# Kernel optimization log

Measured on AMD Instinct MI355X. Metric: run time of the kernel, lower is better.

## Reference

```python
import jax, jax.numpy as jnp
import numpy as np
import math

BOUND = 1e-06
PI = math.pi

N_DIMS = 256
N_ROWS = 524288
DELTA = 1e-06


def _make_buffers(n_dims, delta, radius, scaling, range_type="bound"):
    if range_type == "whole":
        phi_L = 0.0
    else:  # 'bound'
        L = 0.01
        upper_bound = PI / 2 * (1.0 - L)
        phi_L = math.asin(delta ** (1.0 / n_dims))
        phi_L = phi_L if phi_L < upper_bound else upper_bound
    # W_theta: identity with last row duplicated -> (n_dims+1, n_dims)
    eye = np.eye(n_dims, dtype=np.float32)
    W_theta = np.concatenate([eye, eye[-1:]], axis=0)
    # W_phi: strictly upper-triangular ones, with [-2, -1] zeroed
    W_phi = np.triu(np.ones((n_dims + 1, n_dims + 1), dtype=np.float32), k=1)
    W_phi[-2, -1] = 0.0
    b_phi = np.zeros(n_dims + 1, dtype=np.float32)
    b_phi[-1] = -PI / 2.0
    return (
        jnp.float32(phi_L),
        jnp.asarray(W_theta),
        jnp.asarray(W_phi),
        jnp.asarray(b_phi),
        jnp.float32(radius),
        jnp.float32(scaling),
    )


def setup_inputs() -> dict:
    key = jax.random.key(0)
    x = jax.random.normal(key, (N_ROWS, N_DIMS), dtype=jnp.float32)
    phi_L, W_theta, W_phi, b_phi, radius, scaling = _make_buffers(
        N_DIMS, DELTA, radius=1.0, scaling=1.0, range_type="bound"
    )
    return {
        "x": x,
        "W_theta": W_theta,
        "W_phi": W_phi,
        "b_phi": b_phi,
        "phi_L": phi_L,
        "radius": radius,
        "scaling": scaling,
    }


def reference(x, W_theta, W_phi, b_phi, phi_L, radius, scaling):
    # Map features to angles in [phi_L, pi/2)
    ang = (PI / 2 - phi_L) * jax.nn.sigmoid(scaling * x) + phi_L
    # Duplicate last angle: [N, n_dims] -> [N, n_dims+1]
    a = jnp.matmul(ang, W_theta.T)
    # log-sin cumulative sum (via strictly-upper-triangular matmul) + log-cos term
    logx = jnp.matmul(jnp.log(jnp.sin(a) + BOUND), W_phi) + jnp.log(
        jnp.cos(a + b_phi) + BOUND
    )
    return radius * jnp.exp(logx)
```

## Files before the change

kernel.cpp:

```cpp
#include <hip/hip_runtime.h>

#define BOUND 1e-6f
#define HALF_PI 1.57079632679489662f

#define UPD_DPP(oldv, srcv, ctrl, rmask)                                        \
  __int_as_float(__builtin_amdgcn_update_dpp(                                   \
      __float_as_int(oldv), __float_as_int(srcv), (ctrl), (rmask), 0xF, false))

__device__ __forceinline__ float wave_incl_prod(float x) {
    x *= UPD_DPP(1.0f, x, 0x111, 0xF);
    x *= UPD_DPP(1.0f, x, 0x112, 0xF);
    x *= UPD_DPP(1.0f, x, 0x114, 0xF);
    x *= UPD_DPP(1.0f, x, 0x118, 0xF);
    x *= UPD_DPP(1.0f, x, 0x142, 0xA);
    x *= UPD_DPP(1.0f, x, 0x143, 0xC);
    return x;
}

__global__ __launch_bounds__(512) void spherize_kernel(
    const float* __restrict__ x,
    const float* __restrict__ p_phiL,
    const float* __restrict__ p_radius,
    const float* __restrict__ p_scaling,
    float* __restrict__ out,
    int n_rows)
{
    __shared__ float lds[32 * 257];

    const float phi_L   = p_phiL[0];
    const float radius  = p_radius[0];
    const float scaling = p_scaling[0];
    const float amp     = HALF_PI - phi_L;

    const int tid  = threadIdx.x;
    const int lane = tid & 63;
    const int wave = tid >> 6;
    const int row0 = blockIdx.x * 32;
    const int wrow = row0 + wave * 4;

    const int nr_blk = min(32, n_rows - row0);
    const int nr_w   = min(4, max(0, n_rows - wrow));

    float4 xv[4];
    const float* xb = x + (size_t)wrow * 256 + lane * 4;
    #pragma unroll
    for (int i = 0; i < 4; ++i)
        if (i < nr_w) xv[i] = *reinterpret_cast<const float4*>(xb + i * 256);

    #pragma unroll
    for (int i = 0; i < 4; ++i) {
        if (i >= nr_w) break;
        const float* xp = &xv[i].x;
        float s[4], c[4];
        #pragma unroll
        for (int k = 0; k < 4; ++k) {
            float e  = __expf(-scaling * xp[k]);
            float sg = __builtin_amdgcn_rcpf(1.0f + e);
            float a  = fmaf(amp, sg, phi_L);
            s[k] = __sinf(a) + BOUND;
            c[k] = __cosf(a) + BOUND;
        }
        float q1 = s[0];
        float q2 = q1 * s[1];
        float q3 = q2 * s[2];
        float t  = q3 * s[3];
        float scan = wave_incl_prod(t);
        float excl = __shfl_up(scan, 1, 64);
        float base = radius * ((lane == 0) ? 1.0f : excl);

        float* lrow = lds + (wave * 4 + i) * 257 + lane * 4;
        lrow[0] = base * c[0];
        lrow[1] = base * q1 * c[1];
        lrow[2] = base * q2 * c[2];
        lrow[3] = base * q3 * c[3];
        if (lane == 63)
            lrow[4] = radius * scan;
    }
    __syncthreads();

    float* obase = out + (size_t)row0 * 257;
    if (nr_blk == 32) {
        const float4* l4 = reinterpret_cast<const float4*>(lds);
        float4*       o4 = reinterpret_cast<float4*>(obase);
        o4[tid]        = l4[tid];
        o4[tid + 512]  = l4[tid + 512];
        o4[tid + 1024] = l4[tid + 1024];
        o4[tid + 1536] = l4[tid + 1536];
        if (tid < 8) o4[tid + 2048] = l4[tid + 2048];
    } else {
        const int nd = nr_blk * 257;
        for (int i = tid; i < nd; i += 512) obase[i] = lds[i];
    }
}

extern "C" void kernel_launch(void* const* d_in, const int* in_sizes, int n_in,
                              void* d_out, int out_size, void* d_ws, size_t ws_size,
                              hipStream_t stream) {
    const float* x         = (const float*)d_in[0];
    const float* p_phiL    = (const float*)d_in[4];
    const float* p_radius  = (const float*)d_in[5];
    const float* p_scaling = (const float*)d_in[6];
    float* out = (float*)d_out;

    const int n_rows = in_sizes[0] / 256;
    const int blocks = (n_rows + 31) / 32;

    spherize_kernel<<<blocks, 512, 0, stream>>>(x, p_phiL, p_radius, p_scaling,
                                                out, n_rows);
}
```

Baseline: 208.8 us.

## Use strided per-lane columns with four wave scans and division-based exclusive product

Each lane now handles columns lane + 64k instead of four contiguous columns. Loads become scalar, coalesced across the wave, and LDS writes become stride-1 instead of stride-4. In exchange the scan runs four full DPP wave product scans per row instead of one, and chains segments with readlane. The exclusive product is now formed by dividing the inclusive product by s[k] with a reciprocal and the shuffle is dropped, which adds slight rounding risk.

```diff
diff --git a/kernel.cpp b/kernel.cpp
--- a/kernel.cpp
+++ b/kernel.cpp
@@ -41,40 +41,45 @@
     const int nr_blk = min(32, n_rows - row0);
     const int nr_w   = min(4, max(0, n_rows - wrow));
 
-    float4 xv[4];
-    const float* xb = x + (size_t)wrow * 256 + lane * 4;
+    float xv[4][4];
+    const float* xb = x + (size_t)wrow * 256 + lane;
     #pragma unroll
     for (int i = 0; i < 4; ++i)
-        if (i < nr_w) xv[i] = *reinterpret_cast<const float4*>(xb + i * 256);
+        if (i < nr_w) {
+            #pragma unroll
+            for (int k = 0; k < 4; ++k)
+                xv[i][k] = xb[i * 256 + k * 64];
+        }
 
     #pragma unroll
     for (int i = 0; i < 4; ++i) {
         if (i >= nr_w) break;
-        const float* xp = &xv[i].x;
         float s[4], c[4];
         #pragma unroll
         for (int k = 0; k < 4; ++k) {
-            float e  = __expf(-scaling * xp[k]);
+            float e  = __expf(-scaling * xv[i][k]);
             float sg = __builtin_amdgcn_rcpf(1.0f + e);
             float a  = fmaf(amp, sg, phi_L);
             s[k] = __sinf(a) + BOUND;
             c[k] = __cosf(a) + BOUND;
         }
-        float q1 = s[0];
-        float q2 = q1 * s[1];
-        float q3 = q2 * s[2];
-        float t  = q3 * s[3];
-        float scan = wave_incl_prod(t);
-        float excl = __shfl_up(scan, 1, 64);
-        float base = radius * ((lane == 0) ? 1.0f : excl);
 
-        float* lrow = lds + (wave * 4 + i) * 257 + lane * 4;
-        lrow[0] = base * c[0];
-        lrow[1] = base * q1 * c[1];
-        lrow[2] = base * q2 * c[2];
-        lrow[3] = base * q3 * c[3];
+        float incl[4];
+        #pragma unroll
+        for (int k = 0; k < 4; ++k) incl[k] = wave_incl_prod(s[k]);
+
+        float U = radius;
+        float* lrow = lds + (wave * 4 + i) * 257 + lane;
+        #pragma unroll
+        for (int k = 0; k < 4; ++k) {
+            float excl = incl[k] * __builtin_amdgcn_rcpf(s[k]);
+            lrow[64 * k] = U * excl * c[k];
+            float T = __int_as_float(
+                __builtin_amdgcn_readlane(__float_as_int(incl[k]), 63));
+            U *= T;
+        }
         if (lane == 63)
-            lrow[4] = radius * scan;
+            lrow[256 - 63] = U;
     }
     __syncthreads();
 
```

After: 209.9 us. No clear change (+0.5%).
